# Performance work log

Hardware: AMD Instinct MI355X
Metric: run time of the kernel (lower is better)

Reference implementation:

```python
import jax, jax.numpy as jnp
import numpy as np
from jax import lax

B, C_IN, T = 1024, 9, 2048
RT = T // 4            # reduced timesteps after two MaxPool(2)
HID, OUT = 128, 64
N_NODES = B * RT


def _chain_edges(rt, batch):
    """Bidirectional chain graph per sample, offset per batch element (PyG fallback)."""
    i = np.arange(rt - 1)
    src = np.concatenate([i, i + 1])   # edge_index[0] = source j
    dst = np.concatenate([i + 1, i])   # edge_index[1] = target i
    off = (np.arange(batch) * rt)[:, None]
    src = (src[None, :] + off).reshape(-1)
    dst = (dst[None, :] + off).reshape(-1)
    # degree with self-loops (GCNConv adds self-loops): endpoints 2, interior 3
    deg = np.full(rt, 3.0, np.float32)
    deg[0] = deg[-1] = 2.0
    deg = np.tile(deg, batch)
    return jnp.asarray(src, jnp.int32), jnp.asarray(dst, jnp.int32), jnp.asarray(deg ** -0.5)


def _conv1d(x, w, b):
    # x: [B, Cin, T], w: [Cout, Cin, 5] -> [B, Cout, T] (padding=2)
    y = lax.conv_general_dilated(x, w, window_strides=(1,), padding=[(2, 2)],
                                 dimension_numbers=('NCH', 'OIH', 'NCH'))
    return y + b[None, :, None]


def _maxpool2(x):
    b, c, t = x.shape
    return x.reshape(b, c, t // 2, 2).max(axis=-1)


def _gcn(x, W, b, src, dst, dinv):
    # GCNConv: x' = D^-1/2 (A+I) D^-1/2 (x W) + b
    h = x @ W                                        # [N, F]
    norm_e = (dinv[src] * dinv[dst])[:, None]        # per-edge sym norm
    agg = jax.ops.segment_sum(h[src] * norm_e, dst, num_segments=h.shape[0])
    return agg + h * (dinv * dinv)[:, None] + b      # self-loop term: 1/deg


def setup_inputs() -> dict:
    key = jax.random.key(0)
    ks = jax.random.split(key, 12)
    s = lambda k, shp, sc: jax.random.normal(k, shp, jnp.float32) * sc
    return {
        'x': jax.random.normal(ks[0], (B, C_IN, T), jnp.float32),
        'conv1_w': s(ks[1], (16, C_IN, 5), 0.15), 'conv1_b': jnp.zeros((16,), jnp.float32),
        'conv2_w': s(ks[2], (32, 16, 5), 0.1),   'conv2_b': jnp.zeros((32,), jnp.float32),
        'gcn1_w': s(ks[3], (32, HID), 0.17),     'gcn1_b': jnp.zeros((HID,), jnp.float32),
        'gcn2_w': s(ks[4], (HID, HID), 0.09),    'gcn2_b': jnp.zeros((HID,), jnp.float32),
        'fc_w': s(ks[5], (HID, OUT), 0.09),      'fc_b': jnp.zeros((OUT,), jnp.float32),
    }


def reference(x, conv1_w, conv1_b, conv2_w, conv2_b,
              gcn1_w, gcn1_b, gcn2_w, gcn2_b, fc_w, fc_b):
    b, c, t = x.shape
    h = _maxpool2(jax.nn.relu(_conv1d(x, conv1_w, conv1_b)))   # [B,16,T/2]
    h = _maxpool2(jax.nn.relu(_conv1d(h, conv2_w, conv2_b)))   # [B,32,T/4]
    rt = h.shape[-1]
    h = jnp.transpose(h, (0, 2, 1)).reshape(b * rt, 32)        # [N,32]
    src, dst, dinv = _chain_edges(rt, b)
    h = jax.nn.relu(_gcn(h, gcn1_w, gcn1_b, src, dst, dinv))
    h = jax.nn.relu(_gcn(h, gcn2_w, gcn2_b, src, dst, dinv))
    h = h.reshape(b, rt, -1).mean(axis=1)                      # [B,HID]
    return h @ fc_w + fc_b                                     # [B,OUT]
```

## Files before the change

kernel.cpp:

```cpp
#include <hip/hip_runtime.h>
#include <hip/hip_bf16.h>

#define B_      1024
#define CIN     9
#define T0_     2048
#define C1_     16
#define T1_     1024
#define C2_     32
#define RT_     512
#define NNODES  (B_ * RT_)
#define HID_    128
#define OUTF_   64

typedef __attribute__((ext_vector_type(8))) __bf16 bf16x8;
typedef __attribute__((ext_vector_type(4))) float f32x4;
typedef __attribute__((ext_vector_type(8))) unsigned short us8;

__device__ __forceinline__ float bf2f(unsigned short u) {
    union { unsigned int i; float f; } c; c.i = ((unsigned int)u) << 16; return c.f;
}
__device__ __forceinline__ unsigned short f2bf(float f) {
    union { float f; unsigned int i; } c; c.f = f;
    unsigned int i = c.i + 0x7FFFu + ((c.i >> 16) & 1u);
    return (unsigned short)(i >> 16);
}
__device__ __forceinline__ float dinv_of(int r) {
    return (r == 0 || r == RT_ - 1) ? 0.70710678118f : 0.57735026919f;
}

__global__ __launch_bounds__(256) void repack_w(
    const float* __restrict__ W1g, const float* __restrict__ W2g,
    const float* __restrict__ Wc1g, const float* __restrict__ Wc2g,
    unsigned short* __restrict__ Wb1, unsigned short* __restrict__ Wb2,
    unsigned short* __restrict__ Wc1, unsigned short* __restrict__ Wc2)
{
    const int tid = threadIdx.x;
    if (blockIdx.x == 0) {
        for (int e = tid; e < 8 * 64 * 8; e += 256) {
            int j = e & 7, lane = (e >> 3) & 63, ft = e >> 9;
            int k = (lane >> 4) * 8 + j, f = ft * 16 + (lane & 15);
            Wb1[e] = f2bf(W1g[k * 128 + f]);
        }
    } else if (blockIdx.x == 1) {
        for (int e = tid; e < 4 * 8 * 64 * 8; e += 256) {
            int j = e & 7, lane = (e >> 3) & 63, ct = (e >> 9) & 7, ks = e >> 12;
            int k = ks * 32 + (lane >> 4) * 8 + j, f = ct * 16 + (lane & 15);
            Wb2[e] = f2bf(W2g[k * 128 + f]);
        }
    } else if (blockIdx.x == 2) {
        for (int e = tid; e < 3 * 64 * 8; e += 256) {
            int j = e & 7, lane = (e >> 3) & 63, ks = e >> 9;
            int kk = ks * 32 + (lane >> 4) * 8 + j;
            int k = kk >> 4, ci = kk & 15, co = lane & 15;
            Wc1[e] = (k < 5 && ci < CIN) ? f2bf(Wc1g[(co * CIN + ci) * 5 + k]) : 0;
        }
    } else {
        for (int e = tid; e < 3 * 2 * 64 * 8; e += 256) {
            int j = e & 7, lane = (e >> 3) & 63, nt = (e >> 9) & 1, ks = e >> 10;
            int kk = ks * 32 + (lane >> 4) * 8 + j;
            int k = kk >> 4, ci = kk & 15, co = nt * 16 + (lane & 15);
            Wc2[e] = (k < 5) ? f2bf(Wc2g[(co * C1_ + ci) * 5 + k]) : 0;
        }
    }
}

__global__ __launch_bounds__(256) void conv1_mfma(
    const float* __restrict__ x, const unsigned short* __restrict__ Wc1,
    const float* __restrict__ bias, unsigned short* __restrict__ y1t)
{
    __shared__ unsigned short xs[1030 * 24];
    const int tid = threadIdx.x;
    const int chunk = blockIdx.x;
    const int b = blockIdx.y;
    const int t0 = chunk * 1024;
    const float* xb = x + (size_t)b * CIN * T0_;

    for (int s = tid; s < 1030; s += 256) {
        const int t = t0 - 2 + s;
        us8 o0, o1;
        if (t >= 0 && t < T0_) {
            #pragma unroll
            for (int ci = 0; ci < 8; ci++) o0[ci] = f2bf(xb[ci * T0_ + t]);
            o1[0] = f2bf(xb[8 * T0_ + t]);
            #pragma unroll
            for (int jj = 1; jj < 8; jj++) o1[jj] = 0;
        } else {
            #pragma unroll
            for (int jj = 0; jj < 8; jj++) { o0[jj] = 0; o1[jj] = 0; }
        }
        *(us8*)(xs + s * 24) = o0;
        *(us8*)(xs + s * 24 + 8) = o1;
    }
    __syncthreads();

    const int lane = tid & 63, wave = tid >> 6;
    const int m = lane & 15, q = lane >> 4;
    bf16x8 wf[3];
    #pragma unroll
    for (int ks = 0; ks < 3; ks++)
        wf[ks] = *(const bf16x8*)(Wc1 + (ks * 64 + lane) * 8);
    const float bv = bias[m];

    for (int i = 0; i < 16; i++) {
        const int mt = wave * 16 + i;
        f32x4 acc = {};
        #pragma unroll
        for (int ks = 0; ks < 3; ks++) {
            const int row = mt * 16 + m + ks * 2 + (q >> 1);
            const bf16x8 af = *(const bf16x8*)(xs + row * 24 + (q & 1) * 8);
            acc = __builtin_amdgcn_mfma_f32_16x16x32_bf16(af, wf[ks], acc, 0, 0, 0);
        }
        const int tp = chunk * 512 + mt * 8 + q * 2;
        unsigned short* yr = y1t + ((size_t)b * 1024 + tp) * 16 + m;
        const float p0 = fmaxf(fmaxf(acc[0] + bv, 0.f), fmaxf(acc[1] + bv, 0.f));
        const float p1 = fmaxf(fmaxf(acc[2] + bv, 0.f), fmaxf(acc[3] + bv, 0.f));
        yr[0]  = f2bf(p0);
        yr[16] = f2bf(p1);
    }
}

__global__ __launch_bounds__(256) void conv2_mfma(
    const unsigned short* __restrict__ y1t, const unsigned short* __restrict__ Wc2,
    const float* __restrict__ bias, unsigned short* __restrict__ y2t)
{
    __shared__ unsigned short ys[518 * 24];
    const int tid = threadIdx.x;
    const int chunk = blockIdx.x;
    const int b = blockIdx.y;
    const int t0 = chunk * 512;
    const unsigned short* yb = y1t + (size_t)b * 1024 * 16;

    for (int s = tid; s < 518; s += 256) {
        const int t1 = t0 - 2 + s;
        us8 o0, o1;
        if (t1 >= 0 && t1 < 1024) {
            o0 = *(const us8*)(yb + t1 * 16);
            o1 = *(const us8*)(yb + t1 * 16 + 8);
        } else {
            #pragma unroll
            for (int jj = 0; jj < 8; jj++) { o0[jj] = 0; o1[jj] = 0; }
        }
        *(us8*)(ys + s * 24) = o0;
        *(us8*)(ys + s * 24 + 8) = o1;
    }
    __syncthreads();

    const int lane = tid & 63, wave = tid >> 6;
    const int m = lane & 15, q = lane >> 4;
    bf16x8 wf[3][2];
    #pragma unroll
    for (int ks = 0; ks < 3; ks++)
        #pragma unroll
        for (int nt = 0; nt < 2; nt++)
            wf[ks][nt] = *(const bf16x8*)(Wc2 + ((ks * 2 + nt) * 64 + lane) * 8);
    const float bv0 = bias[m], bv1 = bias[16 + m];

    for (int i = 0; i < 8; i++) {
        const int mt = wave * 8 + i;
        f32x4 a0 = {}, a1 = {};
        #pragma unroll
        for (int ks = 0; ks < 3; ks++) {
            const int row = mt * 16 + m + ks * 2 + (q >> 1);
            const bf16x8 af = *(const bf16x8*)(ys + row * 24 + (q & 1) * 8);
            a0 = __builtin_amdgcn_mfma_f32_16x16x32_bf16(af, wf[ks][0], a0, 0, 0, 0);
            a1 = __builtin_amdgcn_mfma_f32_16x16x32_bf16(af, wf[ks][1], a1, 0, 0, 0);
        }
        const int node = chunk * 256 + mt * 8 + q * 2;
        unsigned short* orow = y2t + ((size_t)b * RT_ + node) * 32;
        orow[m]           = f2bf(fmaxf(fmaxf(a0[0] + bv0, 0.f), fmaxf(a0[1] + bv0, 0.f)));
        orow[32 + m]      = f2bf(fmaxf(fmaxf(a0[2] + bv0, 0.f), fmaxf(a0[3] + bv0, 0.f)));
        orow[16 + m]      = f2bf(fmaxf(fmaxf(a1[0] + bv1, 0.f), fmaxf(a1[1] + bv1, 0.f)));
        orow[32 + 16 + m] = f2bf(fmaxf(fmaxf(a1[2] + bv1, 0.f), fmaxf(a1[3] + bv1, 0.f)));
    }
}

__global__ __launch_bounds__(256, 2) void gcn_fused(
    const unsigned short* __restrict__ X,
    const unsigned short* __restrict__ Wb1,
    const unsigned short* __restrict__ Wb2,
    const float* __restrict__ b1,
    const float* __restrict__ b2,
    float* __restrict__ partials)
{
    __shared__ __align__(16) unsigned char lds[75296];
    unsigned short* As1 = (unsigned short*)lds;
    unsigned short* A2  = (unsigned short*)lds;
    unsigned short* H   = (unsigned short*)(lds + 38912);
    float* bls1 = (float*)(lds + 74272);
    float* bls2 = (float*)(lds + 74784);

    const int tid = threadIdx.x;
    const int n0 = blockIdx.x * 128, r0 = n0 & (RT_ - 1);
    if (tid < 128) { bls1[tid] = b1[tid]; bls2[tid] = b2[tid]; }

    for (int s = tid; s < 288; s += 256) {
        const int i = s >> 1, fh = (s & 1) * 16;
        unsigned short* dst = As1 + i * 40 + fh;
        const int r = r0 - 1 + i;
        if (i >= 130 || r < 0 || r >= RT_) {
            us8 z;
            #pragma unroll
            for (int j = 0; j < 8; j++) z[j] = 0;
            *(us8*)dst = z; *(us8*)(dst + 8) = z;
        } else {
            const float dm = dinv_of(r), cm = dm * dm;
            const unsigned short* Xc = X + (size_t)(n0 - 1 + i) * 32 + fh;
            us8 c0 = *(const us8*)(Xc), c1 = *(const us8*)(Xc + 8);
            float v[16];
            #pragma unroll
            for (int j = 0; j < 8; j++) { v[j] = cm * bf2f(c0[j]); v[8 + j] = cm * bf2f(c1[j]); }
            if (r > 0) {
                const float cl = dm * dinv_of(r - 1);
                us8 a0 = *(const us8*)(Xc - 32), a1 = *(const us8*)(Xc - 24);
                #pragma unroll
                for (int j = 0; j < 8; j++) { v[j] += cl * bf2f(a0[j]); v[8 + j] += cl * bf2f(a1[j]); }
            }
            if (r < RT_ - 1) {
                const float cr = dm * dinv_of(r + 1);
                us8 a0 = *(const us8*)(Xc + 32), a1 = *(const us8*)(Xc + 40);
                #pragma unroll
                for (int j = 0; j < 8; j++) { v[j] += cr * bf2f(a0[j]); v[8 + j] += cr * bf2f(a1[j]); }
            }
            us8 o0, o1;
            #pragma unroll
            for (int j = 0; j < 8; j++) { o0[j] = f2bf(v[j]); o1[j] = f2bf(v[8 + j]); }
            *(us8*)dst = o0; *(us8*)(dst + 8) = o1;
        }
    }
    __syncthreads();

    const int lane = tid & 63, wave = tid >> 6;
    const int m = lane & 15, q = lane >> 4;

    {
        const int ft0 = wave * 2;
        const bf16x8 wf0 = *(const bf16x8*)(Wb1 + (ft0 * 64 + lane) * 8);
        const bf16x8 wf1 = *(const bf16x8*)(Wb1 + ((ft0 + 1) * 64 + lane) * 8);
        const float4 bv0 = *(const float4*)&bls1[ft0 * 16 + q * 4];
        const float4 bv1 = *(const float4*)&bls1[(ft0 + 1) * 16 + q * 4];
        #pragma unroll
        for (int nt = 0; nt < 9; nt++) {
            const bf16x8 bfr = *(const bf16x8*)(As1 + (nt * 16 + m) * 40 + q * 8);
            f32x4 a0 = {}, a1 = {};
            a0 = __builtin_amdgcn_mfma_f32_16x16x32_bf16(wf0, bfr, a0, 0, 0, 0);
            a1 = __builtin_amdgcn_mfma_f32_16x16x32_bf16(wf1, bfr, a1, 0, 0, 0);
            const int row = nt * 16 + m;
            if (row < 130) {
                ushort4 o0, o1;
                o0.x = f2bf(fmaxf(a0[0] + bv0.x, 0.f));
                o0.y = f2bf(fmaxf(a0[1] + bv0.y, 0.f));
                o0.z = f2bf(fmaxf(a0[2] + bv0.z, 0.f));
                o0.w = f2bf(fmaxf(a0[3] + bv0.w, 0.f));
                o1.x = f2bf(fmaxf(a1[0] + bv1.x, 0.f));
                o1.y = f2bf(fmaxf(a1[1] + bv1.y, 0.f));
                o1.z = f2bf(fmaxf(a1[2] + bv1.z, 0.f));
                o1.w = f2bf(fmaxf(a1[3] + bv1.w, 0.f));
                *(ushort4*)(H + row * 136 + ft0 * 16 + q * 4) = o0;
                *(ushort4*)(H + row * 136 + (ft0 + 1) * 16 + q * 4) = o1;
            }
        }
    }
    __syncthreads();

    {
        const int j = tid >> 1, fh = (tid & 1) * 64;
        const int r = r0 + j;
        const float dm = dinv_of(r), cm = dm * dm;
        const float cl = (r > 0) ? dm * dinv_of(r - 1) : 0.f;
        const float cr = (r < RT_ - 1) ? dm * dinv_of(r + 1) : 0.f;
        const unsigned short* Hl = H + j * 136 + fh;
        const unsigned short* Hc = Hl + 136;
        const unsigned short* Hr = Hc + 136;
        unsigned short* dst = A2 + j * 152 + fh;
        #pragma unroll
        for (int c = 0; c < 8; c++) {
            us8 cc = *(const us8*)(Hc + c * 8);
            us8 ll = *(const us8*)(Hl + c * 8);
            us8 rr = *(const us8*)(Hr + c * 8);
            us8 o;
            #pragma unroll
            for (int e = 0; e < 8; e++)
                o[e] = f2bf(cm * bf2f(cc[e]) + cl * bf2f(ll[e]) + cr * bf2f(rr[e]));
            *(us8*)(dst + c * 8) = o;
        }
    }
    __syncthreads();

    bf16x8 bw[4][2];
    #pragma unroll
    for (int ks = 0; ks < 4; ks++)
        #pragma unroll
        for (int i = 0; i < 2; i++) {
            int ct = wave * 2 + i;
            bw[ks][i] = *(const bf16x8*)(Wb2 + ((size_t)((ks * 8 + ct) * 64 + lane)) * 8);
        }
    f32x4 acc[8][2] = {};
    #pragma unroll
    for (int ks = 0; ks < 4; ks++) {
        #pragma unroll
        for (int nt = 0; nt < 8; nt++) {
            const bf16x8 af = *(const bf16x8*)(A2 + (nt * 16 + m) * 152 + ks * 32 + q * 8);
            acc[nt][0] = __builtin_amdgcn_mfma_f32_16x16x32_bf16(af, bw[ks][0], acc[nt][0], 0, 0, 0);
            acc[nt][1] = __builtin_amdgcn_mfma_f32_16x16x32_bf16(af, bw[ks][1], acc[nt][1], 0, 0, 0);
        }
    }
    const float bb0 = bls2[wave * 32 + m];
    const float bb1 = bls2[wave * 32 + 16 + m];
    float s0 = 0.f, s1 = 0.f;
    #pragma unroll
    for (int nt = 0; nt < 8; nt++)
        #pragma unroll
        for (int rgi = 0; rgi < 4; rgi++) {
            s0 += fmaxf(acc[nt][0][rgi] + bb0, 0.f);
            s1 += fmaxf(acc[nt][1][rgi] + bb1, 0.f);
        }
    s0 += __shfl_xor(s0, 16, 64); s0 += __shfl_xor(s0, 32, 64);
    s1 += __shfl_xor(s1, 16, 64); s1 += __shfl_xor(s1, 32, 64);
    if (lane < 16) {
        const int batch = n0 >> 9, tile = (n0 >> 7) & 3;
        float* p = partials + ((batch << 2) + tile) * 128 + wave * 32;
        p[m] = s0;
        p[16 + m] = s1;
    }
}

__global__ __launch_bounds__(128) void fc_kernel(
    const float* __restrict__ partials, const float* __restrict__ fw,
    const float* __restrict__ fb, float* __restrict__ out)
{
    __shared__ float sm[128];
    const int b = blockIdx.x, tid = threadIdx.x;
    float s = 0.f;
    #pragma unroll
    for (int t = 0; t < 4; t++) s += partials[((b << 2) + t) * 128 + tid];
    sm[tid] = s * (1.0f / 512.0f);
    __syncthreads();
    if (tid < 64) {
        float acc = fb[tid];
        #pragma unroll 8
        for (int f = 0; f < 128; f++) acc += sm[f] * fw[f * 64 + tid];
        out[b * 64 + tid] = acc;
    }
}

extern "C" void kernel_launch(void* const* d_in, const int* in_sizes, int n_in,
                              void* d_out, int out_size, void* d_ws, size_t ws_size,
                              hipStream_t stream)
{
    const float* x   = (const float*)d_in[0];
    const float* w1  = (const float*)d_in[1];
    const float* b1  = (const float*)d_in[2];
    const float* w2  = (const float*)d_in[3];
    const float* b2  = (const float*)d_in[4];
    const float* g1w = (const float*)d_in[5];
    const float* g1b = (const float*)d_in[6];
    const float* g2w = (const float*)d_in[7];
    const float* g2b = (const float*)d_in[8];
    const float* fw  = (const float*)d_in[9];
    const float* fb  = (const float*)d_in[10];

    char* ws = (char*)d_ws;
    const size_t MB = 1024 * 1024;
    unsigned short* y1t = (unsigned short*)(ws);
    unsigned short* y2t = (unsigned short*)(ws + 32 * MB);
    float* partials     = (float*)(ws + 64 * MB);
    unsigned short* Wb1 = (unsigned short*)(ws + 66 * MB);
    unsigned short* Wb2 = (unsigned short*)(ws + 66 * MB + 64 * 1024);
    unsigned short* Wc1 = (unsigned short*)(ws + 66 * MB + 128 * 1024);
    unsigned short* Wc2 = (unsigned short*)(ws + 66 * MB + 192 * 1024);
    float* out = (float*)d_out;

    repack_w<<<4, 256, 0, stream>>>(g1w, g2w, w1, w2, Wb1, Wb2, Wc1, Wc2);
    conv1_mfma<<<dim3(2, B_), 256, 0, stream>>>(x, Wc1, b1, y1t);
    conv2_mfma<<<dim3(2, B_), 256, 0, stream>>>(y1t, Wc2, b2, y2t);
    gcn_fused<<<NNODES / 128, 256, 0, stream>>>(y2t, Wb1, Wb2, g1b, g2b, partials);
    fc_kernel<<<B_, 128, 0, stream>>>(partials, fw, fb, out);
}
```

Before: 228.1 us.

## Fuse conv1, conv2 and GCN into one kernel with halo recompute in LDS

Merges the two conv kernels and the fused GCN kernel into a single kernel. Each 128-node tile recomputes conv1 and conv2 over a small halo directly from x, keeping intermediates in LDS. This removes the global round trips of y1t and y2t and two kernel launches. In exchange it adds halo recompute, more LDS per block, and extra syncs. The weight repack is also spread over more blocks with coalesced reads of the source weights.

```diff
diff --git a/kernel.cpp b/kernel.cpp
--- a/kernel.cpp
+++ b/kernel.cpp
@@ -5,7 +5,6 @@
 #define CIN     9
 #define T0_     2048
 #define C1_     16
-#define T1_     1024
 #define C2_     32
 #define RT_     512
 #define NNODES  (B_ * RT_)
@@ -35,19 +34,24 @@
     unsigned short* __restrict__ Wc1, unsigned short* __restrict__ Wc2)
 {
     const int tid = threadIdx.x;
-    if (blockIdx.x == 0) {
-        for (int e = tid; e < 8 * 64 * 8; e += 256) {
-            int j = e & 7, lane = (e >> 3) & 63, ft = e >> 9;
-            int k = (lane >> 4) * 8 + j, f = ft * 16 + (lane & 15);
-            Wb1[e] = f2bf(W1g[k * 128 + f]);
-        }
-    } else if (blockIdx.x == 1) {
-        for (int e = tid; e < 4 * 8 * 64 * 8; e += 256) {
-            int j = e & 7, lane = (e >> 3) & 63, ct = (e >> 9) & 7, ks = e >> 12;
-            int k = ks * 32 + (lane >> 4) * 8 + j, f = ct * 16 + (lane & 15);
-            Wb2[e] = f2bf(W2g[k * 128 + f]);
-        }
-    } else if (blockIdx.x == 2) {
+    const int bid = blockIdx.x;
+    if (bid == 0) {
+        for (int s = tid; s < 32 * 128; s += 256) {
+            int k = s >> 7, f = s & 127;
+            int lane = ((k >> 3) << 4) + (f & 15);
+            int e = (((f >> 4) * 64) + lane) * 8 + (k & 7);
+            Wb1[e] = f2bf(W1g[s]);
+        }
+    } else if (bid <= 4) {
+        const int s0 = (bid - 1) * 4096;
+        for (int i = tid; i < 4096; i += 256) {
+            int s = s0 + i;
+            int k = s >> 7, f = s & 127;
+            int ks = k >> 5, lane = (((k >> 3) & 3) << 4) + (f & 15);
+            int e = ((ks * 8 + (f >> 4)) * 64 + lane) * 8 + (k & 7);
+            Wb2[e] = f2bf(W2g[s]);
+        }
+    } else if (bid == 5) {
         for (int e = tid; e < 3 * 64 * 8; e += 256) {
             int j = e & 7, lane = (e >> 3) & 63, ks = e >> 9;
             int kk = ks * 32 + (lane >> 4) * 8 + j;
@@ -64,134 +68,113 @@
     }
 }
 
-__global__ __launch_bounds__(256) void conv1_mfma(
-    const float* __restrict__ x, const unsigned short* __restrict__ Wc1,
-    const float* __restrict__ bias, unsigned short* __restrict__ y1t)
+__global__ __launch_bounds__(256, 2) void mega(
+    const float* __restrict__ x,
+    const unsigned short* __restrict__ Wc1,
+    const unsigned short* __restrict__ Wc2,
+    const unsigned short* __restrict__ Wb1,
+    const unsigned short* __restrict__ Wb2,
+    const float* __restrict__ c1b, const float* __restrict__ c2b,
+    const float* __restrict__ g1b, const float* __restrict__ g2b,
+    float* __restrict__ partials)
 {
-    __shared__ unsigned short xs[1030 * 24];
+    __shared__ __align__(16) unsigned char lds[75808];
+    unsigned short* xs    = (unsigned short*)(lds);
+    unsigned short* As1   = (unsigned short*)(lds);
+    unsigned short* y2loc = (unsigned short*)(lds + 11520);
+    unsigned short* A2    = (unsigned short*)(lds);
+    unsigned short* y1ext = (unsigned short*)(lds + 39424);
+    unsigned short* H     = (unsigned short*)(lds + 39424);
+    float* bls1 = (float*)(lds + 74784);
+    float* bls2 = (float*)(lds + 75296);
+
     const int tid = threadIdx.x;
-    const int chunk = blockIdx.x;
-    const int b = blockIdx.y;
-    const int t0 = chunk * 1024;
-    const float* xb = x + (size_t)b * CIN * T0_;
-
-    for (int s = tid; s < 1030; s += 256) {
-        const int t = t0 - 2 + s;
-        us8 o0, o1;
-        if (t >= 0 && t < T0_) {
-            #pragma unroll
-            for (int ci = 0; ci < 8; ci++) o0[ci] = f2bf(xb[ci * T0_ + t]);
-            o1[0] = f2bf(xb[8 * T0_ + t]);
-            #pragma unroll
-            for (int jj = 1; jj < 8; jj++) o1[jj] = 0;
-        } else {
-            #pragma unroll
-            for (int jj = 0; jj < 8; jj++) { o0[jj] = 0; o1[jj] = 0; }
-        }
-        *(us8*)(xs + s * 24) = o0;
-        *(us8*)(xs + s * 24 + 8) = o1;
-    }
-    __syncthreads();
+    const int b = blockIdx.x >> 2;
+    const int r0 = (blockIdx.x & 3) * 128;
+    const int n0 = blockIdx.x * 128;
+    if (tid < 128) { bls1[tid] = g1b[tid]; bls2[tid] = g2b[tid]; }
 
     const int lane = tid & 63, wave = tid >> 6;
     const int m = lane & 15, q = lane >> 4;
-    bf16x8 wf[3];
-    #pragma unroll
-    for (int ks = 0; ks < 3; ks++)
-        wf[ks] = *(const bf16x8*)(Wc1 + (ks * 64 + lane) * 8);
-    const float bv = bias[m];
-
-    for (int i = 0; i < 16; i++) {
-        const int mt = wave * 16 + i;
-        f32x4 acc = {};
-        #pragma unroll
-        for (int ks = 0; ks < 3; ks++) {
-            const int row = mt * 16 + m + ks * 2 + (q >> 1);
-            const bf16x8 af = *(const bf16x8*)(xs + row * 24 + (q & 1) * 8);
-            acc = __builtin_amdgcn_mfma_f32_16x16x32_bf16(af, wf[ks], acc, 0, 0, 0);
-        }
-        const int tp = chunk * 512 + mt * 8 + q * 2;
-        unsigned short* yr = y1t + ((size_t)b * 1024 + tp) * 16 + m;
-        const float p0 = fmaxf(fmaxf(acc[0] + bv, 0.f), fmaxf(acc[1] + bv, 0.f));
-        const float p1 = fmaxf(fmaxf(acc[2] + bv, 0.f), fmaxf(acc[3] + bv, 0.f));
-        yr[0]  = f2bf(p0);
-        yr[16] = f2bf(p1);
-    }
-}
-
-__global__ __launch_bounds__(256) void conv2_mfma(
-    const unsigned short* __restrict__ y1t, const unsigned short* __restrict__ Wc2,
-    const float* __restrict__ bias, unsigned short* __restrict__ y2t)
-{
-    __shared__ unsigned short ys[518 * 24];
-    const int tid = threadIdx.x;
-    const int chunk = blockIdx.x;
-    const int b = blockIdx.y;
-    const int t0 = chunk * 512;
-    const unsigned short* yb = y1t + (size_t)b * 1024 * 16;
-
-    for (int s = tid; s < 518; s += 256) {
-        const int t1 = t0 - 2 + s;
-        us8 o0, o1;
-        if (t1 >= 0 && t1 < 1024) {
-            o0 = *(const us8*)(yb + t1 * 16);
-            o1 = *(const us8*)(yb + t1 * 16 + 8);
-        } else {
-            #pragma unroll
-            for (int jj = 0; jj < 8; jj++) { o0[jj] = 0; o1[jj] = 0; }
-        }
-        *(us8*)(ys + s * 24) = o0;
-        *(us8*)(ys + s * 24 + 8) = o1;
-    }
-    __syncthreads();
-
-    const int lane = tid & 63, wave = tid >> 6;
-    const int m = lane & 15, q = lane >> 4;
-    bf16x8 wf[3][2];
-    #pragma unroll
-    for (int ks = 0; ks < 3; ks++)
-        #pragma unroll
-        for (int nt = 0; nt < 2; nt++)
-            wf[ks][nt] = *(const bf16x8*)(Wc2 + ((ks * 2 + nt) * 64 + lane) * 8);
-    const float bv0 = bias[m], bv1 = bias[16 + m];
-
-    for (int i = 0; i < 8; i++) {
-        const int mt = wave * 8 + i;
-        f32x4 a0 = {}, a1 = {};
-        #pragma unroll
-        for (int ks = 0; ks < 3; ks++) {
-            const int row = mt * 16 + m + ks * 2 + (q >> 1);
-            const bf16x8 af = *(const bf16x8*)(ys + row * 24 + (q & 1) * 8);
-            a0 = __builtin_amdgcn_mfma_f32_16x16x32_bf16(af, wf[ks][0], a0, 0, 0, 0);
-            a1 = __builtin_amdgcn_mfma_f32_16x16x32_bf16(af, wf[ks][1], a1, 0, 0, 0);
-        }
-        const int node = chunk * 256 + mt * 8 + q * 2;
-        unsigned short* orow = y2t + ((size_t)b * RT_ + node) * 32;
-        orow[m]           = f2bf(fmaxf(fmaxf(a0[0] + bv0, 0.f), fmaxf(a0[1] + bv0, 0.f)));
-        orow[32 + m]      = f2bf(fmaxf(fmaxf(a0[2] + bv0, 0.f), fmaxf(a0[3] + bv0, 0.f)));
-        orow[16 + m]      = f2bf(fmaxf(fmaxf(a1[0] + bv1, 0.f), fmaxf(a1[1] + bv1, 0.f)));
-        orow[32 + 16 + m] = f2bf(fmaxf(fmaxf(a1[2] + bv1, 0.f), fmaxf(a1[3] + bv1, 0.f)));
-    }
-}
-
-__global__ __launch_bounds__(256, 2) void gcn_fused(
-    const unsigned short* __restrict__ X,
-    const unsigned short* __restrict__ Wb1,
-    const unsigned short* __restrict__ Wb2,
-    const float* __restrict__ b1,
-    const float* __restrict__ b2,
-    float* __restrict__ partials)
-{
-    __shared__ __align__(16) unsigned char lds[75296];
-    unsigned short* As1 = (unsigned short*)lds;
-    unsigned short* A2  = (unsigned short*)lds;
-    unsigned short* H   = (unsigned short*)(lds + 38912);
-    float* bls1 = (float*)(lds + 74272);
-    float* bls2 = (float*)(lds + 74784);
-
-    const int tid = threadIdx.x;
-    const int n0 = blockIdx.x * 128, r0 = n0 & (RT_ - 1);
-    if (tid < 128) { bls1[tid] = b1[tid]; bls2[tid] = b2[tid]; }
+
+    {
+        const float* xb = x + (size_t)b * CIN * T0_;
+        const int xbase = 4 * r0 - 14;
+        for (int s = tid; s < 552; s += 256) {
+            const int xt = xbase + s;
+            us8 o0, o1;
+            if (xt >= 0 && xt < T0_) {
+                #pragma unroll
+                for (int ci = 0; ci < 8; ci++) o0[ci] = f2bf(xb[ci * T0_ + xt]);
+                o1[0] = f2bf(xb[8 * T0_ + xt]);
+                #pragma unroll
+                for (int jj = 1; jj < 8; jj++) o1[jj] = 0;
+            } else {
+                #pragma unroll
+                for (int jj = 0; jj < 8; jj++) { o0[jj] = 0; o1[jj] = 0; }
+            }
+            *(us8*)(xs + s * 24) = o0;
+            *(us8*)(xs + s * 24 + 8) = o1;
+        }
+    }
+    __syncthreads();
+
+    {
+        bf16x8 wf[3];
+        #pragma unroll
+        for (int ks = 0; ks < 3; ks++) wf[ks] = *(const bf16x8*)(Wc1 + (ks * 64 + lane) * 8);
+        const float bv = c1b[m];
+        const int t1base = 2 * r0 - 6;
+        for (int mt = wave; mt < 34; mt += 4) {
+            f32x4 acc = {};
+            #pragma unroll
+            for (int ks = 0; ks < 3; ks++) {
+                const int row = mt * 16 + m + ks * 2 + (q >> 1);
+                const bf16x8 af = *(const bf16x8*)(xs + row * 24 + (q & 1) * 8);
+                acc = __builtin_amdgcn_mfma_f32_16x16x32_bf16(af, wf[ks], acc, 0, 0, 0);
+            }
+            const int prow = mt * 8 + q * 2;
+            const int t1a = t1base + prow, t1b = t1a + 1;
+            const float p0 = fmaxf(fmaxf(acc[0], acc[1]) + bv, 0.f);
+            const float p1 = fmaxf(fmaxf(acc[2], acc[3]) + bv, 0.f);
+            if (prow < 268)
+                y1ext[prow * 16 + m] = (t1a >= 0 && t1a < 1024) ? f2bf(p0) : (unsigned short)0;
+            if (prow + 1 < 268)
+                y1ext[(prow + 1) * 16 + m] = (t1b >= 0 && t1b < 1024) ? f2bf(p1) : (unsigned short)0;
+        }
+        for (int idx = tid; idx < 192; idx += 256) y1ext[268 * 16 + idx] = 0;
+    }
+    __syncthreads();
+
+    {
+        bf16x8 wf[3][2];
+        #pragma unroll
+        for (int ks = 0; ks < 3; ks++)
+            #pragma unroll
+            for (int nt = 0; nt < 2; nt++)
+                wf[ks][nt] = *(const bf16x8*)(Wc2 + ((ks * 2 + nt) * 64 + lane) * 8);
+        const float bv0 = c2b[m], bv1 = c2b[16 + m];
+        for (int mt = wave; mt < 17; mt += 4) {
+            f32x4 a0 = {}, a1 = {};
+            #pragma unroll
+            for (int ks = 0; ks < 3; ks++) {
+                const int row = mt * 16 + m + ks * 2 + (q >> 1);
+                const bf16x8 af = *(const bf16x8*)(y1ext + row * 16 + (q & 1) * 8);
+                a0 = __builtin_amdgcn_mfma_f32_16x16x32_bf16(af, wf[ks][0], a0, 0, 0, 0);
+                a1 = __builtin_amdgcn_mfma_f32_16x16x32_bf16(af, wf[ks][1], a1, 0, 0, 0);
+            }
+            const int nrow = mt * 8 + q * 2;
+            if (nrow < 132) {
+                y2loc[nrow * 32 + m]      = f2bf(fmaxf(fmaxf(a0[0], a0[1]) + bv0, 0.f));
+                y2loc[nrow * 32 + 16 + m] = f2bf(fmaxf(fmaxf(a1[0], a1[1]) + bv1, 0.f));
+            }
+            if (nrow + 1 < 132) {
+                y2loc[(nrow + 1) * 32 + m]      = f2bf(fmaxf(fmaxf(a0[2], a0[3]) + bv0, 0.f));
+                y2loc[(nrow + 1) * 32 + 16 + m] = f2bf(fmaxf(fmaxf(a1[2], a1[3]) + bv1, 0.f));
+            }
+        }
+    }
+    __syncthreads();
 
     for (int s = tid; s < 288; s += 256) {
         const int i = s >> 1, fh = (s & 1) * 16;
@@ -204,20 +187,20 @@
             *(us8*)dst = z; *(us8*)(dst + 8) = z;
         } else {
             const float dm = dinv_of(r), cm = dm * dm;
-            const unsigned short* Xc = X + (size_t)(n0 - 1 + i) * 32 + fh;
-            us8 c0 = *(const us8*)(Xc), c1 = *(const us8*)(Xc + 8);
+            const unsigned short* Yc = y2loc + (i + 1) * 32 + fh;
+            us8 c0 = *(const us8*)(Yc), c1 = *(const us8*)(Yc + 8);
             float v[16];
             #pragma unroll
             for (int j = 0; j < 8; j++) { v[j] = cm * bf2f(c0[j]); v[8 + j] = cm * bf2f(c1[j]); }
             if (r > 0) {
                 const float cl = dm * dinv_of(r - 1);
-                us8 a0 = *(const us8*)(Xc - 32), a1 = *(const us8*)(Xc - 24);
+                us8 a0 = *(const us8*)(Yc - 32), a1 = *(const us8*)(Yc - 24);
                 #pragma unroll
                 for (int j = 0; j < 8; j++) { v[j] += cl * bf2f(a0[j]); v[8 + j] += cl * bf2f(a1[j]); }
             }
             if (r < RT_ - 1) {
                 const float cr = dm * dinv_of(r + 1);
-                us8 a0 = *(const us8*)(Xc + 32), a1 = *(const us8*)(Xc + 40);
+                us8 a0 = *(const us8*)(Yc + 32), a1 = *(const us8*)(Yc + 40);
                 #pragma unroll
                 for (int j = 0; j < 8; j++) { v[j] += cr * bf2f(a0[j]); v[8 + j] += cr * bf2f(a1[j]); }
             }
@@ -228,9 +211,6 @@
         }
     }
     __syncthreads();
-
-    const int lane = tid & 63, wave = tid >> 6;
-    const int m = lane & 15, q = lane >> 4;
 
     {
         const int ft0 = wave * 2;
@@ -317,8 +297,7 @@
     s0 += __shfl_xor(s0, 16, 64); s0 += __shfl_xor(s0, 32, 64);
     s1 += __shfl_xor(s1, 16, 64); s1 += __shfl_xor(s1, 32, 64);
     if (lane < 16) {
-        const int batch = n0 >> 9, tile = (n0 >> 7) & 3;
-        float* p = partials + ((batch << 2) + tile) * 128 + wave * 32;
+        float* p = partials + (size_t)blockIdx.x * 128 + wave * 32;
         p[m] = s0;
         p[16 + m] = s1;
     }
@@ -361,18 +340,15 @@
 
     char* ws = (char*)d_ws;
     const size_t MB = 1024 * 1024;
-    unsigned short* y1t = (unsigned short*)(ws);
-    unsigned short* y2t = (unsigned short*)(ws + 32 * MB);
-    float* partials     = (float*)(ws + 64 * MB);
-    unsigned short* Wb1 = (unsigned short*)(ws + 66 * MB);
-    unsigned short* Wb2 = (unsigned short*)(ws + 66 * MB + 64 * 1024);
-    unsigned short* Wc1 = (unsigned short*)(ws + 66 * MB + 128 * 1024);
-    unsigned short* Wc2 = (unsigned short*)(ws + 66 * MB + 192 * 1024);
+    float* partials     = (float*)(ws);
+    unsigned short* Wb1 = (unsigned short*)(ws + 2 * MB);
+    unsigned short* Wb2 = (unsigned short*)(ws + 2 * MB + 16 * 1024);
+    unsigned short* Wc1 = (unsigned short*)(ws + 2 * MB + 64 * 1024);
+    unsigned short* Wc2 = (unsigned short*)(ws + 2 * MB + 80 * 1024);
     float* out = (float*)d_out;
 
-    repack_w<<<4, 256, 0, stream>>>(g1w, g2w, w1, w2, Wb1, Wb2, Wc1, Wc2);
-    conv1_mfma<<<dim3(2, B_), 256, 0, stream>>>(x, Wc1, b1, y1t);
-    conv2_mfma<<<dim3(2, B_), 256, 0, stream>>>(y1t, Wc2, b2, y2t);
-    gcn_fused<<<NNODES / 128, 256, 0, stream>>>(y2t, Wb1, Wb2, g1b, g2b, partials);
+    repack_w<<<7, 256, 0, stream>>>(g1w, g2w, w1, w2, Wb1, Wb2, Wc1, Wc2);
+    mega<<<NNODES / 128, 256, 0, stream>>>(x, Wc1, Wc2, Wb1, Wb2,
+                                           b1, b2, g1b, g2b, partials);
     fc_kernel<<<B_, 128, 0, stream>>>(partials, fw, fb, out);
 }
```

Result: faster. 215.2 us (-5.7%).
